# Kernel optimization log

Hardware: AMD Instinct MI355X
Metric: run time of the kernel (lower is better)

The kernel has to match this reference:

```python
import jax, jax.numpy as jnp
import numpy as np

B, N, D = 4, 2048, 768
H, DH = 12, 64  # heads, qk/v head dim
SCALE = DH ** -0.5


def setup_inputs() -> dict:
    key = jax.random.key(0)
    ks = jax.random.split(key, 6)
    s = (1.0 / np.sqrt(D)).astype(np.float32)
    return {
        'x': jax.random.normal(ks[0], (B, N, D), dtype=jnp.float32),
        'x_mask': jax.random.randint(ks[1], (B, N), 0, 2) > 0,
        'Wq': jax.random.normal(ks[2], (D, H * DH), dtype=jnp.float32) * s,
        'Wk': jax.random.normal(ks[3], (D, H * DH), dtype=jnp.float32) * s,
        'Wv': jax.random.normal(ks[4], (D, H * DH), dtype=jnp.float32) * s,
        'Wo': jax.random.normal(ks[5], (H * DH, D), dtype=jnp.float32) * s,
    }


def reference(x, x_mask, Wq, Wk, Wv, Wo):
    # projections (no bias), split heads: b n (h d) -> b h n d
    q = (x @ Wq).reshape(B, N, H, DH).transpose(0, 2, 1, 3)
    k = (x @ Wk).reshape(B, N, H, DH).transpose(0, 2, 1, 3)
    v = (x @ Wv).reshape(B, N, H, DH).transpose(0, 2, 1, 3)
    dots = jnp.einsum('bhid,bhjd->bhij', q, k) * SCALE
    mask_value = -jnp.finfo(dots.dtype).max
    # q_mask [b,1,i,1] & k_mask [b,1,1,j] (self-attention: both from x_mask)
    input_mask = x_mask[:, None, :, None] & x_mask[:, None, None, :]
    dots = jnp.where(input_mask, dots, mask_value)
    attn = jax.nn.softmax(dots.astype(jnp.float32), axis=-1)
    # dropout is identity in eval mode
    out = jnp.einsum('bhij,bhjd->bhid', attn, v)
    out = out.transpose(0, 2, 1, 3).reshape(B, N, H * DH)  # b h n d -> b n (h d)
    return out @ Wo
```

## Files before the change

### kernel.cpp

```cpp
#include <hip/hip_runtime.h>


#define B_ 4
#define N_ 2048
#define D_ 768
#define H_ 12
#define DH_ 64
#define CSC_ 0.18033688011112042f

typedef __attribute__((ext_vector_type(8))) short bf8_t;
typedef __attribute__((ext_vector_type(4))) float f4_t;
typedef __attribute__((ext_vector_type(16))) float f16v;
typedef __attribute__((ext_vector_type(4))) int i4_t;

__device__ __forceinline__ short f2b(float f) {
  union { float f; unsigned u; } v; v.f = f;
  unsigned r = v.u + 0x7FFFu + ((v.u >> 16) & 1u);
  return (short)(r >> 16);
}
__device__ __forceinline__ float b2f(short s) {
  union { unsigned u; float f; } v; v.u = ((unsigned)(unsigned short)s) << 16;
  return v.f;
}
__device__ __forceinline__ unsigned cvtpk(float lo, float hi) {
  unsigned r;
  asm("v_cvt_pk_bf16_f32 %0, %1, %2" : "=v"(r) : "v"(lo), "v"(hi));
  return r;
}
__device__ __forceinline__ void plswap(unsigned& a, unsigned& b) {
  asm("v_permlane32_swap_b32 %0, %1" : "+v"(a), "+v"(b));
}
__device__ __forceinline__ float max3f(float a, float b, float c) {
  float r;
  asm("v_max3_f32 %0, %1, %2, %3" : "=v"(r) : "v"(a), "v"(b), "v"(c));
  return r;
}

#define GLOAD_LDS16(gp, lp)                                                       \
  __builtin_amdgcn_global_load_lds(                                               \
      (const __attribute__((address_space(1))) void*)(gp),                        \
      (__attribute__((address_space(3))) void*)(lp), 16, 0, 0)

__global__ __launch_bounds__(256) void k_convx(const float* __restrict__ x,
                                               short* __restrict__ xb) {
  int i = blockIdx.x * 256 + threadIdx.x;
  int base = i * 8;
  float4 a = *(const float4*)(x + base);
  float4 b = *(const float4*)(x + base + 4);
  bf8_t v;
  v[0] = f2b(a.x); v[1] = f2b(a.y); v[2] = f2b(a.z); v[3] = f2b(a.w);
  v[4] = f2b(b.x); v[5] = f2b(b.y); v[6] = f2b(b.z); v[7] = f2b(b.w);
  *(bf8_t*)(xb + base) = v;
}

__global__ __launch_bounds__(256) void k_wtrans(const float* __restrict__ Wq,
                                                const float* __restrict__ Wk,
                                                const float* __restrict__ Wv,
                                                const float* __restrict__ Wo,
                                                short* __restrict__ WqkvT,
                                                short* __restrict__ WoT) {
  int z = blockIdx.z;
  const float* W = (z == 0) ? Wq : (z == 1) ? Wk : (z == 2) ? Wv : Wo;
  short* dst = (z < 3) ? (WqkvT + (size_t)z * D_ * D_) : WoT;
  float sc = (z == 0) ? CSC_ : 1.f;
  __shared__ float T[64][65];
  int r0 = blockIdx.y * 64, c0 = blockIdx.x * 64;
  int tr = threadIdx.x >> 6, tc = threadIdx.x & 63;
#pragma unroll
  for (int i = 0; i < 16; ++i) {
    int r = tr + i * 4;
    T[r][tc] = W[(size_t)(r0 + r) * D_ + c0 + tc];
  }
  __syncthreads();
#pragma unroll
  for (int i = 0; i < 16; ++i) {
    int r = tr + i * 4;
    dst[(size_t)(c0 + r) * D_ + r0 + tc] = f2b(T[tc][r] * sc);
  }
}

template <int MODE>
__global__ __launch_bounds__(256) void k_gemm(const short* __restrict__ A,
                                              const short* __restrict__ BT, int K,
                                              short* __restrict__ Qb, short* __restrict__ Kb,
                                              short* __restrict__ Vb,
                                              float* __restrict__ Cout, int ldc) {
  __shared__ short As[128 * 72];
  __shared__ short Bs[128 * 72];
  int row0 = blockIdx.y * 128, col0 = blockIdx.x * 128;
  int tid = threadIdx.x, lane = tid & 63, w = tid >> 6;
  int wr = w >> 1, wc = w & 1;
  int lr = lane & 15, lhi = lane >> 4;
  f4_t acc[4][4];
#pragma unroll
  for (int mi = 0; mi < 4; ++mi)
#pragma unroll
    for (int ni = 0; ni < 4; ++ni) acc[mi][ni] = (f4_t){0.f, 0.f, 0.f, 0.f};

  for (int k0 = 0; k0 < K; k0 += 64) {
    __syncthreads();
#pragma unroll
    for (int cc = 0; cc < 4; ++cc) {
      int c = tid + cc * 256;
      int r = c >> 3, c8 = (c & 7) * 8;
      *(bf8_t*)(As + r * 72 + c8) = *(const bf8_t*)(A + (size_t)(row0 + r) * K + k0 + c8);
    }
#pragma unroll
    for (int cc = 0; cc < 4; ++cc) {
      int c = tid + cc * 256;
      int r = c >> 3, c8 = (c & 7) * 8;
      *(bf8_t*)(Bs + r * 72 + c8) = *(const bf8_t*)(BT + (size_t)(col0 + r) * K + k0 + c8);
    }
    __syncthreads();
#pragma unroll
    for (int kc = 0; kc < 2; ++kc) {
      bf8_t av[4], bv[4];
#pragma unroll
      for (int mi = 0; mi < 4; ++mi)
        av[mi] = *(const bf8_t*)(As + (64 * wr + 16 * mi + lr) * 72 + kc * 32 + lhi * 8);
#pragma unroll
      for (int ni = 0; ni < 4; ++ni)
        bv[ni] = *(const bf8_t*)(Bs + (64 * wc + 16 * ni + lr) * 72 + kc * 32 + lhi * 8);
#pragma unroll
      for (int mi = 0; mi < 4; ++mi)
#pragma unroll
        for (int ni = 0; ni < 4; ++ni)
          acc[mi][ni] = __builtin_amdgcn_mfma_f32_16x16x32_bf16(av[mi], bv[ni], acc[mi][ni], 0, 0, 0);
    }
  }
#pragma unroll
  for (int mi = 0; mi < 4; ++mi)
#pragma unroll
    for (int ni = 0; ni < 4; ++ni)
#pragma unroll
      for (int r = 0; r < 4; ++r) {
        int row = row0 + 64 * wr + 16 * mi + 4 * lhi + r;
        int col = col0 + 64 * wc + 16 * ni + lr;
        float v = acc[mi][ni][r];
        if (MODE == 0) {
          int which = col / 768;
          int cc2 = col - which * 768;
          int h = cc2 >> 6, dh = cc2 & 63;
          int b = row >> 11, n = row & 2047;
          size_t dst = (((size_t)(b * H_ + h)) * N_ + n) * DH_ + dh;
          short bv2 = f2b(v);
          if (which == 0) Qb[dst] = bv2;
          else if (which == 1) Kb[dst] = bv2;
          else Vb[dst] = bv2;
        } else {
          Cout[(size_t)row * ldc + col] = v;
        }
      }
}

__global__ __launch_bounds__(256) void k_maskidx(const int* __restrict__ xmask,
                                                 int* __restrict__ idx,
                                                 int* __restrict__ cnt) {
  int b = blockIdx.x, t = threadIdx.x;
  const int* mp = xmask + b * N_;
  int loc[8], c = 0;
#pragma unroll
  for (int j = 0; j < 8; ++j) {
    int n = t * 8 + j;
    if (mp[n]) loc[c++] = n;
  }
  __shared__ int sc[256];
  sc[t] = c;
  __syncthreads();
  for (int off = 1; off < 256; off <<= 1) {
    int v = (t >= off) ? sc[t - off] : 0;
    __syncthreads();
    sc[t] += v;
    __syncthreads();
  }
  int base = sc[t] - c;
  int* op = idx + b * N_;
  for (int j = 0; j < c; ++j) op[base + j] = loc[j];
  if (t == 255) cnt[b] = sc[255];
}

__global__ __launch_bounds__(256) void k_vmeanA(const short* __restrict__ Vb,
                                                float* __restrict__ part) {
  int bh = blockIdx.y, ch = blockIdx.x, t = threadIdx.x;
  int rg = t >> 3, cg = t & 7;
  const short* vp = Vb + ((size_t)bh * N_ + ch * 256 + rg) * DH_ + cg * 8;
  float a[8] = {0, 0, 0, 0, 0, 0, 0, 0};
#pragma unroll
  for (int k = 0; k < 8; ++k) {
    bf8_t v = *(const bf8_t*)(vp + (size_t)32 * k * DH_);
#pragma unroll
    for (int e = 0; e < 8; ++e) a[e] += b2f(v[e]);
  }
  __shared__ float red[8][32][8];
#pragma unroll
  for (int e = 0; e < 8; ++e) red[cg][rg][e] = a[e];
  __syncthreads();
  if (t < 64) {
    int g = t >> 3, j = t & 7;
    float s = 0;
#pragma unroll
    for (int i = 0; i < 32; ++i) s += red[g][i][j];
    part[((size_t)bh * 8 + ch) * 64 + g * 8 + j] = s;
  }
}

__global__ __launch_bounds__(256) void k_vmeanB(const float* __restrict__ part,
                                                float* __restrict__ Vmean) {
  int i = blockIdx.x * 256 + threadIdx.x;
  if (i >= 48 * 64) return;
  int bh = i >> 6, dh = i & 63;
  float s = 0;
#pragma unroll
  for (int c = 0; c < 8; ++c) s += part[((size_t)bh * 8 + c) * 64 + dh];
  Vmean[i] = s * (1.f / 2048.f);
}

__global__ __launch_bounds__(256) void k_gather(const short* __restrict__ Kb,
                                                const short* __restrict__ Vb,
                                                const int* __restrict__ idx,
                                                const int* __restrict__ cnt,
                                                short* __restrict__ Kc,
                                                short* __restrict__ Vtc) {
  int bh = blockIdx.y, b = bh / H_;
  int j0 = blockIdx.x * 64;
  int cn = cnt[b];
  int cp = (cn + 63) & ~63;
  if (j0 >= cp) return;
  int t = threadIdx.x;
  __shared__ int sidx[64];
  __shared__ short vt[64][72];
  if (t < 64) sidx[t] = (j0 + t < cn) ? idx[b * N_ + j0 + t] : -1;
  __syncthreads();
  int r = t >> 2, c16 = (t & 3) * 16;
  int src = sidx[r];
  const bf8_t zz = {0, 0, 0, 0, 0, 0, 0, 0};
#pragma unroll
  for (int u = 0; u < 2; ++u) {
    bf8_t kv = (src >= 0) ? *(const bf8_t*)(Kb + ((size_t)bh * N_ + src) * DH_ + c16 + u * 8) : zz;
    bf8_t vv = (src >= 0) ? *(const bf8_t*)(Vb + ((size_t)bh * N_ + src) * DH_ + c16 + u * 8) : zz;
    *(bf8_t*)(Kc + ((size_t)bh * N_ + j0 + r) * DH_ + c16 + u * 8) = kv;
    *(bf8_t*)(&vt[r][c16 + u * 8]) = vv;
  }
  __syncthreads();
  int dh = t >> 2;
#pragma unroll
  for (int u = 0; u < 2; ++u) {
    bf8_t ov;
#pragma unroll
    for (int e = 0; e < 8; ++e) ov[e] = vt[c16 + u * 8 + e][dh];
    *(bf8_t*)(Vtc + ((size_t)bh * DH_ + dh) * N_ + j0 + c16 + u * 8) = ov;
  }
}

__global__ __launch_bounds__(256) void k_fill(const int* __restrict__ xmask,
                                              const float* __restrict__ Vmean,
                                              short* __restrict__ Ao) {
  int b = blockIdx.y;
  int n = blockIdx.x * 32 + (threadIdx.x >> 3);
  int cg = threadIdx.x & 7;
  if (xmask[b * N_ + n]) return;
#pragma unroll
  for (int k = 0; k < 12; ++k) {
    int col = cg * 8 + k * 64;
    int h = col >> 6, dh = col & 63;
    const float* vp = Vmean + ((size_t)b * H_ + h) * 64 + dh;
    bf8_t ov;
#pragma unroll
    for (int e = 0; e < 8; ++e) ov[e] = f2b(vp[e]);
    *(bf8_t*)(Ao + ((size_t)b * N_ + n) * D_ + col) = ov;
  }
}

__global__ __launch_bounds__(256, 3) void k_attn(const short* __restrict__ Q,
                                                 const short* __restrict__ Kcg,
                                                 const short* __restrict__ Vtcg,
                                                 const int* __restrict__ idx,
                                                 const int* __restrict__ cnt,
                                                 short* __restrict__ Aout) {
  int bh = blockIdx.y;
  int b = bh / H_, h = bh - b * H_;
  int cn = cnt[b];
  int nqt = (cn + 127) >> 7;
  if ((int)blockIdx.x >= nqt) return;
  int nkt = (cn + 63) >> 6;
  const short* Qp = Q + (size_t)bh * N_ * DH_;
  const short* Kp = Kcg + (size_t)bh * N_ * DH_;
  const short* Vp = Vtcg + (size_t)bh * DH_ * N_;
  const int* ip = idx + b * N_;
  int q0 = blockIdx.x * 128;
  int tid = threadIdx.x, lane = tid & 63, w = tid >> 6;
  int lq = lane & 31, hi = lane >> 5;

  __shared__ char smem[32768];

  int qrow = q0 + 32 * w + lq;
  int qn = ip[qrow < cn ? qrow : cn - 1];

  bf8_t qf[4];
#pragma unroll
  for (int kc = 0; kc < 4; ++kc)
    qf[kc] = *(const bf8_t*)(Qp + (size_t)qn * DH_ + 16 * kc + 8 * hi);

  short NEGBIG = f2b(-1e30f);
  bf8_t qbf = {hi ? (short)0 : (short)0x3F80, 0, 0, 0, 0, 0, 0, 0};

  f16v acco[2];
#pragma unroll
  for (int i = 0; i < 16; ++i) { acco[0][i] = 0.f; acco[1][i] = 0.f; }
  float m = -1e29f, lsum = 0.f;

  auto STAGE = [&](int key0, int buf) {
    char* kb_ = smem + buf * 16384;
    char* vb_ = kb_ + 8192;
    int row = tid >> 3;
    int cb = (tid & 7) * 16;
    char* lk = kb_ + ((tid >> 6) << 10);
    char* lv = vb_ + ((tid >> 6) << 10);
#pragma unroll
    for (int rr = 0; rr < 2; ++rr) {
      int r2 = row + rr * 32;
      int sw = cb ^ ((r2 & 7) << 4);
      GLOAD_LDS16((const char*)(Kp + (size_t)(key0 + r2) * DH_) + sw, lk + rr * 4096);
      GLOAD_LDS16((const char*)(Vp + (size_t)r2 * N_ + key0) + sw, lv + rr * 4096);
    }
  };

  STAGE(0, 0);
  __syncthreads();

  for (int kt = 0; kt < nkt; ++kt) {
    int cur = kt & 1;
    if (kt + 1 < nkt) STAGE((kt + 1) * 64, cur ^ 1);

    const char* kbase = smem + cur * 16384;
    const char* vbase = kbase + 8192;
    int key0 = kt * 64;

    f16v accs[2];
#pragma unroll
    for (int i = 0; i < 16; ++i) { accs[0][i] = 0.f; accs[1][i] = 0.f; }
    int swz = (lq & 7) << 4;
    __builtin_amdgcn_s_setprio(1);
#pragma unroll
    for (int kc = 0; kc < 4; ++kc) {
      int colb = (32 * kc + 16 * hi) ^ swz;
      bf8_t k0 = *(const bf8_t*)(kbase + lq * 128 + colb);
      bf8_t k1 = *(const bf8_t*)(kbase + (32 + lq) * 128 + colb);
      accs[0] = __builtin_amdgcn_mfma_f32_32x32x16_bf16(k0, qf[kc], accs[0], 0, 0, 0);
      accs[1] = __builtin_amdgcn_mfma_f32_32x32x16_bf16(k1, qf[kc], accs[1], 0, 0, 0);
    }
    __builtin_amdgcn_s_setprio(0);
    if (key0 + 64 > cn) {
      bf8_t bf0 = {(hi || key0 + lq < cn) ? (short)0 : NEGBIG, 0, 0, 0, 0, 0, 0, 0};
      bf8_t bf1 = {(hi || key0 + 32 + lq < cn) ? (short)0 : NEGBIG, 0, 0, 0, 0, 0, 0, 0};
      accs[0] = __builtin_amdgcn_mfma_f32_32x32x16_bf16(bf0, qbf, accs[0], 0, 0, 0);
      accs[1] = __builtin_amdgcn_mfma_f32_32x32x16_bf16(bf1, qbf, accs[1], 0, 0, 0);
    }

    float mx = max3f(accs[0][0], accs[0][1], accs[0][2]);
#pragma unroll
    for (int i = 3; i < 15; i += 2) mx = max3f(mx, accs[0][i], accs[0][i + 1]);
    mx = max3f(mx, accs[0][15], accs[1][0]);
#pragma unroll
    for (int i = 1; i < 15; i += 2) mx = max3f(mx, accs[1][i], accs[1][i + 1]);
    mx = fmaxf(mx, accs[1][15]);
    mx = fmaxf(mx, __shfl_xor(mx, 32));
    if (!__all(mx <= m + 8.f)) {
      float mnew = fmaxf(m, mx);
      float sc = __builtin_amdgcn_exp2f(m - mnew);
      m = mnew;
      lsum *= sc;
#pragma unroll
      for (int i = 0; i < 16; ++i) { acco[0][i] *= sc; acco[1][i] *= sc; }
    }
    float psa[4] = {0.f, 0.f, 0.f, 0.f};
#pragma unroll
    for (int kb2 = 0; kb2 < 2; ++kb2)
#pragma unroll
      for (int r = 0; r < 16; ++r) {
        float p = __builtin_amdgcn_exp2f(accs[kb2][r] - m);
        accs[kb2][r] = p;
        psa[r & 3] += p;
      }
    float ps = (psa[0] + psa[1]) + (psa[2] + psa[3]);
    ps += __shfl_xor(ps, 32);
    lsum += ps;

    __builtin_amdgcn_s_setprio(1);
#pragma unroll
    for (int kc = 0; kc < 4; ++kc) {
      int kb2 = kc >> 1, rb = (kc & 1) * 8;
      unsigned a_ = cvtpk(accs[kb2][rb + 0], accs[kb2][rb + 1]);
      unsigned b_ = cvtpk(accs[kb2][rb + 4], accs[kb2][rb + 5]);
      unsigned c_ = cvtpk(accs[kb2][rb + 2], accs[kb2][rb + 3]);
      unsigned d_ = cvtpk(accs[kb2][rb + 6], accs[kb2][rb + 7]);
      plswap(a_, b_);
      plswap(c_, d_);
      union { i4_t i; bf8_t v; } pu;
      pu.i = (i4_t){(int)a_, (int)c_, (int)b_, (int)d_};
      int colb = (32 * kc + 16 * hi) ^ swz;
      bf8_t v0 = *(const bf8_t*)(vbase + lq * 128 + colb);
      bf8_t v1 = *(const bf8_t*)(vbase + (32 + lq) * 128 + colb);
      acco[0] = __builtin_amdgcn_mfma_f32_32x32x16_bf16(v0, pu.v, acco[0], 0, 0, 0);
      acco[1] = __builtin_amdgcn_mfma_f32_32x32x16_bf16(v1, pu.v, acco[1], 0, 0, 0);
    }
    __builtin_amdgcn_s_setprio(0);

    __syncthreads();
  }
  __syncthreads();

  float inv = 1.f / lsum;
  unsigned* Os = (unsigned*)smem + w * 1152;
#pragma unroll
  for (int dhb = 0; dhb < 2; ++dhb)
#pragma unroll
    for (int r = 0; r < 16; r += 2) {
      unsigned pk = cvtpk(acco[dhb][r] * inv, acco[dhb][r + 1] * inv);
      int colu = 16 * dhb + ((r & 3) >> 1) + 4 * (r >> 2) + 2 * hi;
      Os[lq * 36 + colu] = pk;
    }
#pragma unroll
  for (int it = 0; it < 4; ++it) {
    int q = (lane >> 3) + 8 * it;
    int qr2 = q0 + 32 * w + q;
    if (qr2 < cn) {
      int n = ip[qr2];
      i4_t vv = *(const i4_t*)(Os + q * 36 + 4 * (lane & 7));
      union { i4_t i; bf8_t s; } u2;
      u2.i = vv;
      size_t off = ((size_t)b * N_ + n) * D_ + h * DH_ + 8 * (lane & 7);
      *(bf8_t*)(Aout + off) = u2.s;
    }
  }
}

extern "C" void kernel_launch(void* const* d_in, const int* in_sizes, int n_in,
                              void* d_out, int out_size, void* d_ws, size_t ws_size,
                              hipStream_t stream) {
  (void)in_sizes; (void)n_in; (void)out_size; (void)ws_size;
  const float* x  = (const float*)d_in[0];
  const int*   xm = (const int*)d_in[1];
  const float* Wq = (const float*)d_in[2];
  const float* Wk = (const float*)d_in[3];
  const float* Wv = (const float*)d_in[4];
  const float* Wo = (const float*)d_in[5];
  float* out = (float*)d_out;
  char* ws = (char*)d_ws;

  short* x_bf  = (short*)(ws + 0);
  short* Ao    = (short*)(ws + 0);
  short* WqkvT = (short*)(ws + 12582912);
  int*   idxb  = (int*)(ws + 12582912);
  int*   cntb  = (int*)(ws + 12615680);
  float* part  = (float*)(ws + 12615744);
  float* Vmean = (float*)(ws + 12714048);
  short* WoT   = (short*)(ws + 16121856);
  short* Qb    = (short*)(ws + 17301504);
  short* Kb    = (short*)(ws + 29884416);
  short* Vb    = (short*)(ws + 42467328);
  short* Kc    = (short*)(ws + 55050240);
  short* Vtc   = (short*)(ws + 67633152);

  k_convx<<<3072, 256, 0, stream>>>(x, x_bf);
  k_wtrans<<<dim3(12, 12, 4), 256, 0, stream>>>(Wq, Wk, Wv, Wo, WqkvT, WoT);
  k_gemm<0><<<dim3(18, 64), 256, 0, stream>>>(x_bf, WqkvT, 768, Qb, Kb, Vb, nullptr, 0);
  k_maskidx<<<4, 256, 0, stream>>>(xm, idxb, cntb);
  k_vmeanA<<<dim3(8, 48), 256, 0, stream>>>(Vb, part);
  k_vmeanB<<<12, 256, 0, stream>>>(part, Vmean);
  k_gather<<<dim3(32, 48), 256, 0, stream>>>(Kb, Vb, idxb, cntb, Kc, Vtc);
  k_attn<<<dim3(16, 48), 256, 0, stream>>>(Qb, Kc, Vtc, idxb, cntb, Ao);
  k_fill<<<dim3(64, 4), 256, 0, stream>>>(xm, Vmean, Ao);
  k_gemm<1><<<dim3(6, 64), 256, 0, stream>>>(Ao, WoT, 768, nullptr, nullptr, nullptr, out, 768);
}
```

Measured before the change: 142.7 us.

## Double-buffer GEMM tiles with direct global-to-LDS loads, XOR swizzle, and block remap

The projection GEMM now uses two LDS buffers per operand and fills them with direct global-to-LDS 16-byte loads (GLOAD_LDS16), prefetching the next K tile while MFMAs consume the current one. LDS rows drop the 72-element padding and use an XOR swizzle to avoid bank conflicts. Workgroup indices are remapped across eight groups, likely to spread tiles across XCDs for cache locality. This removes the per-iteration load-then-sync stall at the cost of doubled LDS use. It relies on a GLOAD_LDS16 macro defined in the unseen part of the file and on the grid size being divisible by 8.

```diff
diff --git a/kernel.cpp b/kernel.cpp
--- a/kernel.cpp
+++ b/kernel.cpp
@@ -85,9 +85,15 @@
                                               short* __restrict__ Qb, short* __restrict__ Kb,
                                               short* __restrict__ Vb,
                                               float* __restrict__ Cout, int ldc) {
-  __shared__ short As[128 * 72];
-  __shared__ short Bs[128 * 72];
-  int row0 = blockIdx.y * 128, col0 = blockIdx.x * 128;
+  __shared__ short As[2][128 * 64];
+  __shared__ short Bs[2][128 * 64];
+  int gx = gridDim.x;
+  int nwg = gx * gridDim.y;
+  int flat = blockIdx.y * gx + blockIdx.x;
+  int cpx = nwg >> 3;
+  int swzb = (flat & 7) * cpx + (flat >> 3);
+  int row0 = (swzb / gx) * 128, col0 = (swzb % gx) * 128;
+
   int tid = threadIdx.x, lane = tid & 63, w = tid >> 6;
   int wr = w >> 1, wc = w & 1;
   int lr = lane & 15, lhi = lane >> 4;
@@ -97,37 +103,52 @@
 #pragma unroll
     for (int ni = 0; ni < 4; ++ni) acc[mi][ni] = (f4_t){0.f, 0.f, 0.f, 0.f};
 
-  for (int k0 = 0; k0 < K; k0 += 64) {
-    __syncthreads();
-#pragma unroll
-    for (int cc = 0; cc < 4; ++cc) {
-      int c = tid + cc * 256;
-      int r = c >> 3, c8 = (c & 7) * 8;
-      *(bf8_t*)(As + r * 72 + c8) = *(const bf8_t*)(A + (size_t)(row0 + r) * K + k0 + c8);
-    }
-#pragma unroll
-    for (int cc = 0; cc < 4; ++cc) {
-      int c = tid + cc * 256;
-      int r = c >> 3, c8 = (c & 7) * 8;
-      *(bf8_t*)(Bs + r * 72 + c8) = *(const bf8_t*)(BT + (size_t)(col0 + r) * K + k0 + c8);
-    }
-    __syncthreads();
+  int sub = lane >> 3;
+  int scb = ((lane & 7) * 16) ^ (sub << 4);
+  auto STAGE = [&](int k0, int buf) {
+    char* ab = (char*)As[buf] + (w << 12);
+    char* bb = (char*)Bs[buf] + (w << 12);
+#pragma unroll
+    for (int i = 0; i < 4; ++i) {
+      int r = 32 * w + 8 * i + sub;
+      GLOAD_LDS16((const char*)(A + (size_t)(row0 + r) * K + k0) + scb, ab + (i << 10));
+      GLOAD_LDS16((const char*)(BT + (size_t)(col0 + r) * K + k0) + scb, bb + (i << 10));
+    }
+  };
+
+  STAGE(0, 0);
+  __syncthreads();
+
+  int nt = K / 64;
+  for (int t = 0; t < nt; ++t) {
+    int cur = t & 1;
+    if (t + 1 < nt) STAGE((t + 1) * 64, cur ^ 1);
+
+    const char* Ac = (const char*)As[cur];
+    const char* Bc = (const char*)Bs[cur];
+    int rsw = (lr & 7) << 4;
 #pragma unroll
     for (int kc = 0; kc < 2; ++kc) {
       bf8_t av[4], bv[4];
 #pragma unroll
-      for (int mi = 0; mi < 4; ++mi)
-        av[mi] = *(const bf8_t*)(As + (64 * wr + 16 * mi + lr) * 72 + kc * 32 + lhi * 8);
-#pragma unroll
-      for (int ni = 0; ni < 4; ++ni)
-        bv[ni] = *(const bf8_t*)(Bs + (64 * wc + 16 * ni + lr) * 72 + kc * 32 + lhi * 8);
+      for (int mi = 0; mi < 4; ++mi) {
+        int row = 64 * wr + 16 * mi + lr;
+        av[mi] = *(const bf8_t*)(Ac + row * 128 + ((64 * kc + 16 * lhi) ^ rsw));
+      }
+#pragma unroll
+      for (int ni = 0; ni < 4; ++ni) {
+        int row = 64 * wc + 16 * ni + lr;
+        bv[ni] = *(const bf8_t*)(Bc + row * 128 + ((64 * kc + 16 * lhi) ^ rsw));
+      }
 #pragma unroll
       for (int mi = 0; mi < 4; ++mi)
 #pragma unroll
         for (int ni = 0; ni < 4; ++ni)
           acc[mi][ni] = __builtin_amdgcn_mfma_f32_16x16x32_bf16(av[mi], bv[ni], acc[mi][ni], 0, 0, 0);
     }
-  }
+    __syncthreads();
+  }
+
 #pragma unroll
   for (int mi = 0; mi < 4; ++mi)
 #pragma unroll
```

After: 132.1 us. 7.4% less time.
